# Kernel optimization log

Measured on AMD Instinct MI355X. Metric: run time of the kernel, lower is better.

## Reference

```python
import jax, jax.numpy as jnp
import numpy as np

B, LQ, C = 4, 4096, 384
NH, NL, NP = 6, 1, 4
HL, WL = 64, 64
LV = HL * WL
DH = C // NH
EPS = 1e-6


def layer_norm(x, g, b):
    mu = jnp.mean(x, axis=-1, keepdims=True)
    var = jnp.mean(jnp.square(x - mu), axis=-1, keepdims=True)
    return (x - mu) * jax.lax.rsqrt(var + EPS) * g + b


def ms_deform_attn_core(value, spatial_shapes, level_start_index, loc, attn_w):
    # value [B,LV,NH,DH]; loc [B,LQ,NH,NL,NP,2] in [0,1]; attn_w [B,LQ,NH,NL,NP]
    ss = np.asarray(spatial_shapes)
    lsi = np.asarray(level_start_index)
    Bv, _, nH, dh = value.shape
    Lq = loc.shape[1]
    nP = loc.shape[4]
    out = jnp.zeros((Bv, Lq, nH, dh), value.dtype)
    for l in range(loc.shape[3]):
        Hl, Wl = int(ss[l, 0]), int(ss[l, 1])
        st = int(lsi[l])
        vflat = value[:, st:st + Hl * Wl]  # [B, Hl*Wl, nH, dh]
        xy = loc[:, :, :, l]               # [B,LQ,nH,NP,2]
        # grid_sample(align_corners=False): pixel = loc * size - 0.5
        x = xy[..., 0] * Wl - 0.5
        y = xy[..., 1] * Hl - 0.5
        x0 = jnp.floor(x)
        y0 = jnp.floor(y)
        wx = x - x0
        wy = y - y0
        x0i = x0.astype(jnp.int32)
        y0i = y0.astype(jnp.int32)

        def gather(xi, yi):
            # zero padding outside the feature map (padding_mode='zeros')
            valid = (xi >= 0) & (xi < Wl) & (yi >= 0) & (yi < Hl)
            idx = jnp.clip(yi, 0, Hl - 1) * Wl + jnp.clip(xi, 0, Wl - 1)  # [B,LQ,nH,NP]
            idx2 = idx.transpose(0, 1, 3, 2).reshape(Bv, Lq * nP, nH)
            g = jnp.take_along_axis(vflat, idx2[..., None], axis=1)       # [B,LQ*NP,nH,dh]
            g = g.reshape(Bv, Lq, nP, nH, dh).transpose(0, 1, 3, 2, 4)    # [B,LQ,nH,NP,dh]
            return g * valid[..., None].astype(value.dtype)

        samp = (gather(x0i, y0i) * ((1 - wx) * (1 - wy))[..., None]
                + gather(x0i + 1, y0i) * (wx * (1 - wy))[..., None]
                + gather(x0i, y0i + 1) * ((1 - wx) * wy)[..., None]
                + gather(x0i + 1, y0i + 1) * (wx * wy)[..., None])
        out = out + jnp.einsum('bqhpd,bqhp->bqhd', samp, attn_w[:, :, :, l])
    return out.reshape(Bv, Lq, nH * dh)


def setup_inputs() -> dict:
    key = jax.random.key(0)
    ks = jax.random.split(key, 12)
    s = 0.02
    return {
        'query': jax.random.normal(ks[0], (B, LQ, C), jnp.float32),
        'reference_points': jax.random.uniform(ks[1], (B, LQ, NL, 2), dtype=jnp.float32),
        'feat': jax.random.normal(ks[2], (B, LV, C), jnp.float32),
        'spatial_shapes': jnp.array([[HL, WL]], jnp.int32),
        'level_start_index': jnp.array([0], jnp.int32),
        'ln_q_g': jnp.ones((C,), jnp.float32), 'ln_q_b': jnp.zeros((C,), jnp.float32),
        'ln_f_g': jnp.ones((C,), jnp.float32), 'ln_f_b': jnp.zeros((C,), jnp.float32),
        'gamma': jax.random.normal(ks[3], (C,), jnp.float32) * 0.1,
        'Wv': jax.random.normal(ks[4], (C, C), jnp.float32) * s,
        'bv': jnp.zeros((C,), jnp.float32),
        'Wo': jax.random.normal(ks[5], (C, NH * NL * NP * 2), jnp.float32) * s,
        'bo': jax.random.normal(ks[6], (NH * NL * NP * 2,), jnp.float32) * 0.5,
        'Wa': jax.random.normal(ks[7], (C, NH * NL * NP), jnp.float32) * s,
        'ba': jnp.zeros((NH * NL * NP,), jnp.float32),
        'Wout': jax.random.normal(ks[8], (C, C), jnp.float32) * s,
        'bout': jnp.zeros((C,), jnp.float32),
    }


def reference(query, reference_points, feat, spatial_shapes, level_start_index,
              ln_q_g, ln_q_b, ln_f_g, ln_f_b, gamma,
              Wv, bv, Wo, bo, Wa, ba, Wout, bout):
    q = layer_norm(query, ln_q_g, ln_q_b)
    f = layer_norm(feat, ln_f_g, ln_f_b)
    value = (f @ Wv + bv).reshape(B, LV, NH, DH)
    offsets = (q @ Wo + bo).reshape(B, LQ, NH, NL, NP, 2)
    attn_w = jax.nn.softmax((q @ Wa + ba).reshape(B, LQ, NH, NL * NP), axis=-1)
    attn_w = attn_w.reshape(B, LQ, NH, NL, NP)
    # offset normalizer is (W, H) per level
    norm = jnp.stack([spatial_shapes[:, 1], spatial_shapes[:, 0]], -1).astype(jnp.float32)
    loc = reference_points[:, :, None, :, None, :] + offsets / norm[None, None, None, :, None, :]
    attn = ms_deform_attn_core(value, spatial_shapes, level_start_index, loc, attn_w)
    attn = attn @ Wout + bout
    return query + gamma * attn
```

## Files before the change

### kernel.cpp

```cpp
#include <hip/hip_runtime.h>
#include <math.h>

#define B_    4
#define LQ_   4096
#define C_    384
#define NH_   6
#define NP_   4
#define HL_   64
#define WL_   64
#define LV_   (HL_ * WL_)
#define ROWS_ (B_ * LQ_)
#define EPS_  1e-6f
#define NOFF_ 48
#define NLOG_ 24

typedef unsigned short u16;
typedef __bf16 bf16x8 __attribute__((ext_vector_type(8)));
typedef float  f32x4  __attribute__((ext_vector_type(4)));

__device__ __forceinline__ float bf2f(u16 v) {
    unsigned int u = ((unsigned int)v) << 16;
    return __uint_as_float(u);
}
__device__ __forceinline__ u16 f2bf(float f) {
    unsigned int u = __float_as_uint(f);
    u += 0x7fff + ((u >> 16) & 1);
    return (u16)(u >> 16);
}

__device__ __forceinline__ f32x4 mfma16(bf16x8 a, bf16x8 b, f32x4 c) {
    return __builtin_amdgcn_mfma_f32_16x16x32_bf16(a, b, c, 0, 0, 0);
}

__device__ __forceinline__ void gl_lds16(const u16* g, u16* l) {
    __builtin_amdgcn_global_load_lds(
        (const __attribute__((address_space(1))) unsigned int*)g,
        (__attribute__((address_space(3))) unsigned int*)l, 16, 0, 0);
}

__global__ __launch_bounds__(256) void prep_weights(
    const float* __restrict__ Wv, const float* __restrict__ Wout,
    const float* __restrict__ Wo, const float* __restrict__ Wa,
    const float* __restrict__ bo, const float* __restrict__ ba,
    u16* __restrict__ WvT, u16* __restrict__ WoutT, u16* __restrict__ WcT,
    float* __restrict__ bias_c)
{
    const int KN = 384 * 384;
    int idx = blockIdx.x * 256 + threadIdx.x;
    if (idx < KN) {
        int n = idx / 384, k = idx - n * 384;
        WvT[idx] = f2bf(Wv[k * 384 + n]);
    } else if (idx < 2 * KN) {
        int t = idx - KN;
        int n = t / 384, k = t - n * 384;
        WoutT[t] = f2bf(Wout[k * 384 + n]);
    } else if (idx < 2 * KN + 80 * 384) {
        int t = idx - 2 * KN;
        int n = t / 384, k = t - n * 384;
        float v = (n < 48) ? Wo[k * 48 + n] : (n < 72 ? Wa[k * 24 + (n - 48)] : 0.f);
        WcT[t] = f2bf(v);
    } else if (idx < 2 * KN + 80 * 384 + 80) {
        int n = idx - (2 * KN + 80 * 384);
        bias_c[n] = (n < 48) ? bo[n] : (n < 72 ? ba[n - 48] : 0.f);
    }
}

__global__ __launch_bounds__(256) void ln_kernel(
    const float* __restrict__ query, const float* __restrict__ feat,
    const float* __restrict__ qg, const float* __restrict__ qb,
    const float* __restrict__ fg, const float* __restrict__ fb,
    u16* __restrict__ qout, u16* __restrict__ fout)
{
    int wid  = threadIdx.x >> 6;
    int lane = threadIdx.x & 63;
    int row  = blockIdx.x * 4 + wid;
    const float *src, *g, *bsh;
    u16* dst;
    int r;
    if (row < ROWS_) { src = query; g = qg; bsh = qb; dst = qout; r = row; }
    else             { src = feat;  g = fg; bsh = fb; dst = fout; r = row - ROWS_; }

    const float* x = src + (size_t)r * C_;
    float v[6];
    float s = 0.f;
#pragma unroll
    for (int k = 0; k < 6; ++k) { v[k] = x[lane + 64 * k]; s += v[k]; }
#pragma unroll
    for (int off = 32; off; off >>= 1) s += __shfl_xor(s, off);
    float mu = s * (1.f / C_);

    float s2 = 0.f;
#pragma unroll
    for (int k = 0; k < 6; ++k) { float d = v[k] - mu; s2 += d * d; }
#pragma unroll
    for (int off = 32; off; off >>= 1) s2 += __shfl_xor(s2, off);
    float rs = rsqrtf(s2 * (1.f / C_) + EPS_);

    u16* y = dst + (size_t)r * C_;
#pragma unroll
    for (int k = 0; k < 6; ++k) {
        int c = lane + 64 * k;
        y[c] = f2bf((v[k] - mu) * rs * g[c] + bsh[c]);
    }
}

template<int MODE>
__global__ __launch_bounds__(256) void mfma_gemm(
    const u16* __restrict__ A, const u16* __restrict__ Bt,
    const float* __restrict__ bias, const float* __restrict__ resid,
    const float* __restrict__ gamma, void* __restrict__ Cout)
{
    const int K = 384, N = 384;
    __shared__ __align__(16) u16 As[128 * 32];
    __shared__ __align__(16) u16 Bs[128 * 32];

    int tid  = threadIdx.x;
    int lane = tid & 63, wid = tid >> 6;
    int m0 = blockIdx.y * 128, n0 = blockIdx.x * 128;
    int wm = (wid >> 1) * 64, wn = (wid & 1) * 64;
    int fr = lane & 15, quad = lane >> 4;

    int srow = tid >> 2;
    int scol = (tid & 3) * 8;
    const u16* agp0 = A  + (size_t)(m0 + srow) * K + scol;
    const u16* agp1 = A  + (size_t)(m0 + srow + 64) * K + scol;
    const u16* bgp0 = Bt + (size_t)(n0 + srow) * K + scol;
    const u16* bgp1 = Bt + (size_t)(n0 + srow + 64) * K + scol;
    u16* al0 = As + tid * 8;  u16* al1 = As + 2048 + tid * 8;
    u16* bl0 = Bs + tid * 8;  u16* bl1 = Bs + 2048 + tid * 8;

    f32x4 zero = {0.f, 0.f, 0.f, 0.f};
    f32x4 acc[4][4];
#pragma unroll
    for (int i = 0; i < 4; ++i)
#pragma unroll
        for (int j = 0; j < 4; ++j) acc[i][j] = zero;

    for (int k0 = 0; k0 < K; k0 += 32) {
        gl_lds16(agp0 + k0, al0);
        gl_lds16(agp1 + k0, al1);
        gl_lds16(bgp0 + k0, bl0);
        gl_lds16(bgp1 + k0, bl1);
        __syncthreads();
        bf16x8 af[4], bfr[4];
#pragma unroll
        for (int i = 0; i < 4; ++i)
            af[i] = *(bf16x8*)&As[(wm + i * 16 + fr) * 32 + quad * 8];
#pragma unroll
        for (int j = 0; j < 4; ++j)
            bfr[j] = *(bf16x8*)&Bs[(wn + j * 16 + fr) * 32 + quad * 8];
#pragma unroll
        for (int i = 0; i < 4; ++i)
#pragma unroll
            for (int j = 0; j < 4; ++j)
                acc[i][j] = mfma16(af[i], bfr[j], acc[i][j]);
        __syncthreads();
    }

#pragma unroll
    for (int i = 0; i < 4; ++i) {
        int row = m0 + wm + i * 16 + quad * 4;
#pragma unroll
        for (int j = 0; j < 4; ++j) {
            int col = n0 + wn + j * 16 + fr;
            float bcol = bias[col];
#pragma unroll
            for (int r = 0; r < 4; ++r) {
                float v = acc[i][j][r] + bcol;
                size_t o = (size_t)(row + r) * N + col;
                if (MODE == 0) ((u16*)Cout)[o] = f2bf(v);
                else ((float*)Cout)[o] = resid[o] + gamma[col] * v;
            }
        }
    }
}

__global__ __launch_bounds__(256) void mfma_small(
    const u16* __restrict__ A, const u16* __restrict__ Bt,
    const float* __restrict__ bias,
    float* __restrict__ offs, float* __restrict__ logits)
{
    const int K = 384;
    __shared__ __align__(16) u16 Bs[80 * 384];
    __shared__ __align__(16) u16 As[64 * 32];

    int tid  = threadIdx.x;
    int lane = tid & 63, wid = tid >> 6;
    int m0 = blockIdx.x * 64;
    int fr = lane & 15, quad = lane >> 4;

    for (int i = tid; i < 3840; i += 256)
        ((float4*)Bs)[i] = ((const float4*)Bt)[i];

    int srow = tid >> 2, scol = (tid & 3) * 8;
    const u16* agp = A + (size_t)(m0 + srow) * K + scol;
    u16* al = As + tid * 8;

    f32x4 zero = {0.f, 0.f, 0.f, 0.f};
    f32x4 acc[5];
#pragma unroll
    for (int j = 0; j < 5; ++j) acc[j] = zero;

    __syncthreads();

    for (int k0 = 0; k0 < K; k0 += 32) {
        gl_lds16(agp + k0, al);
        __syncthreads();
        bf16x8 af = *(bf16x8*)&As[(wid * 16 + fr) * 32 + quad * 8];
#pragma unroll
        for (int j = 0; j < 5; ++j) {
            bf16x8 bf = *(bf16x8*)&Bs[(j * 16 + fr) * 384 + k0 + quad * 8];
            acc[j] = mfma16(af, bf, acc[j]);
        }
        __syncthreads();
    }

    int row = m0 + wid * 16 + quad * 4;
#pragma unroll
    for (int j = 0; j < 5; ++j) {
        int col = j * 16 + fr;
        if (col < 72) {
            float bcol = bias[col];
#pragma unroll
            for (int r = 0; r < 4; ++r) {
                float v = acc[j][r] + bcol;
                if (col < 48) offs[(size_t)(row + r) * NOFF_ + col] = v;
                else          logits[(size_t)(row + r) * NLOG_ + (col - 48)] = v;
            }
        }
    }
}

__global__ __launch_bounds__(384) void sample_kernel(
    const u16*  __restrict__ value,
    const float* __restrict__ rp,
    const float* __restrict__ offs,
    const float* __restrict__ logits,
    u16* __restrict__ attn)
{
    __shared__ float w_s[NH_][NP_][4];
    __shared__ int   pos_s[NH_][NP_][4];

    int bq = blockIdx.x;
    int b  = bq / LQ_;
    int t  = threadIdx.x;

    if (t < NLOG_) {
        int h = t >> 2, p = t & 3;
        const float* lg = logits + (size_t)bq * NLOG_ + h * 4;
        float l0 = lg[0], l1 = lg[1], l2 = lg[2], l3 = lg[3];
        float mx = fmaxf(fmaxf(l0, l1), fmaxf(l2, l3));
        float e0 = expf(l0 - mx), e1 = expf(l1 - mx), e2 = expf(l2 - mx), e3 = expf(l3 - mx);
        float den = e0 + e1 + e2 + e3;
        float ep = (p == 0) ? e0 : (p == 1) ? e1 : (p == 2) ? e2 : e3;
        float aw = ep / den;

        float rx = rp[(size_t)bq * 2 + 0];
        float ry = rp[(size_t)bq * 2 + 1];
        float ox = offs[(size_t)bq * NOFF_ + t * 2 + 0];
        float oy = offs[(size_t)bq * NOFF_ + t * 2 + 1];
        float x = (rx + ox * (1.0f / WL_)) * (float)WL_ - 0.5f;
        float y = (ry + oy * (1.0f / HL_)) * (float)HL_ - 0.5f;
        float x0f = floorf(x), y0f = floorf(y);
        float wx = x - x0f, wy = y - y0f;
        int x0 = (int)x0f, y0 = (int)y0f;
#pragma unroll
        for (int c = 0; c < 4; ++c) {
            int xi = x0 + (c & 1);
            int yi = y0 + (c >> 1);
            bool valid = (xi >= 0) && (xi < WL_) && (yi >= 0) && (yi < HL_);
            int xc = xi < 0 ? 0 : (xi > WL_ - 1 ? WL_ - 1 : xi);
            int yc = yi < 0 ? 0 : (yi > HL_ - 1 ? HL_ - 1 : yi);
            float wc = ((c & 1) ? wx : 1.f - wx) * ((c >> 1) ? wy : 1.f - wy);
            pos_s[h][p][c] = yc * WL_ + xc;
            w_s[h][p][c]   = valid ? wc * aw : 0.f;
        }
    }
    __syncthreads();

    int h = t >> 6, d = t & 63;
    const u16* vb = value + ((size_t)b * LV_) * C_ + h * 64 + d;
    float acc = 0.f;
#pragma unroll
    for (int p = 0; p < NP_; ++p) {
#pragma unroll
        for (int c = 0; c < 4; ++c) {
            acc += w_s[h][p][c] * bf2f(vb[(size_t)pos_s[h][p][c] * C_]);
        }
    }
    attn[(size_t)bq * C_ + t] = f2bf(acc);
}

extern "C" void kernel_launch(void* const* d_in, const int* in_sizes, int n_in,
                              void* d_out, int out_size, void* d_ws, size_t ws_size,
                              hipStream_t stream)
{
    const float* query  = (const float*)d_in[0];
    const float* rp     = (const float*)d_in[1];
    const float* feat   = (const float*)d_in[2];
    const float* gamma  = (const float*)d_in[9];
    const float* Wv     = (const float*)d_in[10];
    const float* bv     = (const float*)d_in[11];
    const float* Wo     = (const float*)d_in[12];
    const float* bo     = (const float*)d_in[13];
    const float* Wa     = (const float*)d_in[14];
    const float* ba     = (const float*)d_in[15];
    const float* Wout   = (const float*)d_in[16];
    const float* bout   = (const float*)d_in[17];
    float* out = (float*)d_out;

    u16* wsu    = (u16*)d_ws;
    u16* qb     = wsu;
    u16* fb     = qb    + (size_t)ROWS_ * C_;
    u16* valb   = fb    + (size_t)ROWS_ * C_;
    u16* attnb  = valb  + (size_t)ROWS_ * C_;
    u16* WvT    = attnb + (size_t)ROWS_ * C_;
    u16* WoutT  = WvT   + 384 * 384;
    u16* WcT    = WoutT + 384 * 384;
    float* offs   = (float*)(WcT + 80 * 384);
    float* logits = offs + (size_t)ROWS_ * NOFF_;
    float* bias_c = logits + (size_t)ROWS_ * NLOG_;

    prep_weights<<<1273, 256, 0, stream>>>(Wv, Wout, Wo, Wa, bo, ba,
                                           WvT, WoutT, WcT, bias_c);

    ln_kernel<<<8192, 256, 0, stream>>>(query, feat,
        (const float*)d_in[5], (const float*)d_in[6],
        (const float*)d_in[7], (const float*)d_in[8], qb, fb);

    mfma_gemm<0><<<dim3(3, 128), 256, 0, stream>>>(fb, WvT, bv, nullptr, nullptr, valb);

    mfma_small<<<256, 256, 0, stream>>>(qb, WcT, bias_c, offs, logits);

    sample_kernel<<<ROWS_, 384, 0, stream>>>(valb, rp, offs, logits, attnb);

    mfma_gemm<1><<<dim3(3, 128), 256, 0, stream>>>(attnb, WoutT, bout, query, gamma, out);
}
```

Measured before the change: 202.7 us.

## Fuse deformable sampling with output projection GEMM in one kernel

Replaces the per-query sampling kernel and the separate output-projection GEMM with one kernel. Each block takes 32 queries, computes softmax and sampling metadata into shared memory, and gathers value rows with 8-wide bf16 vector loads. The sampled rows stay in LDS and are multiplied by WoutT with MFMA, and the residual epilogue is applied in place. This removes the attn round-trip through global memory and one launch, but WoutT is read straight from global memory by every block with no LDS staging, and the grid is only 512 blocks.

```diff
diff --git a/kernel.cpp b/kernel.cpp
--- a/kernel.cpp
+++ b/kernel.cpp
@@ -104,11 +104,9 @@
     }
 }
 
-template<int MODE>
-__global__ __launch_bounds__(256) void mfma_gemm(
+__global__ __launch_bounds__(256) void mfma_gemm_value(
     const u16* __restrict__ A, const u16* __restrict__ Bt,
-    const float* __restrict__ bias, const float* __restrict__ resid,
-    const float* __restrict__ gamma, void* __restrict__ Cout)
+    const float* __restrict__ bias, u16* __restrict__ Cout)
 {
     const int K = 384, N = 384;
     __shared__ __align__(16) u16 As[128 * 32];
@@ -167,9 +165,7 @@
 #pragma unroll
             for (int r = 0; r < 4; ++r) {
                 float v = acc[i][j][r] + bcol;
-                size_t o = (size_t)(row + r) * N + col;
-                if (MODE == 0) ((u16*)Cout)[o] = f2bf(v);
-                else ((float*)Cout)[o] = resid[o] + gamma[col] * v;
+                Cout[(size_t)(row + r) * N + col] = f2bf(v);
             }
         }
     }
@@ -231,64 +227,135 @@
     }
 }
 
-__global__ __launch_bounds__(384) void sample_kernel(
+#define QT_   32
+#define APAD_ 392
+
+__global__ __launch_bounds__(256) void fused_sample_out(
     const u16*  __restrict__ value,
     const float* __restrict__ rp,
     const float* __restrict__ offs,
     const float* __restrict__ logits,
-    u16* __restrict__ attn)
-{
-    __shared__ float w_s[NH_][NP_][4];
-    __shared__ int   pos_s[NH_][NP_][4];
-
-    int bq = blockIdx.x;
-    int b  = bq / LQ_;
+    const u16*  __restrict__ WoutT,
+    const float* __restrict__ bout,
+    const float* __restrict__ gamma,
+    const float* __restrict__ query,
+    float* __restrict__ out)
+{
+    __shared__ float meta[QT_ * NH_ * NP_ * 4];
+    __shared__ __align__(16) u16 attn_s[QT_ * APAD_];
+
     int t  = threadIdx.x;
-
-    if (t < NLOG_) {
-        int h = t >> 2, p = t & 3;
-        const float* lg = logits + (size_t)bq * NLOG_ + h * 4;
+    int m0 = blockIdx.x * QT_;
+    int b  = m0 / LQ_;
+
+#pragma unroll
+    for (int j = 0; j < 3; ++j) {
+        int u = t + 256 * j;
+        int q = u / (NH_ * NP_);
+        int rem = u - q * (NH_ * NP_);
+        int h = rem >> 2, p = rem & 3;
+        int r = m0 + q;
+
+        const float* lg = logits + (size_t)r * NLOG_ + h * 4;
         float l0 = lg[0], l1 = lg[1], l2 = lg[2], l3 = lg[3];
         float mx = fmaxf(fmaxf(l0, l1), fmaxf(l2, l3));
-        float e0 = expf(l0 - mx), e1 = expf(l1 - mx), e2 = expf(l2 - mx), e3 = expf(l3 - mx);
+        float e0 = expf(l0 - mx), e1 = expf(l1 - mx);
+        float e2 = expf(l2 - mx), e3 = expf(l3 - mx);
         float den = e0 + e1 + e2 + e3;
         float ep = (p == 0) ? e0 : (p == 1) ? e1 : (p == 2) ? e2 : e3;
         float aw = ep / den;
 
-        float rx = rp[(size_t)bq * 2 + 0];
-        float ry = rp[(size_t)bq * 2 + 1];
-        float ox = offs[(size_t)bq * NOFF_ + t * 2 + 0];
-        float oy = offs[(size_t)bq * NOFF_ + t * 2 + 1];
-        float x = (rx + ox * (1.0f / WL_)) * (float)WL_ - 0.5f;
-        float y = (ry + oy * (1.0f / HL_)) * (float)HL_ - 0.5f;
+        float rx = rp[(size_t)r * 2 + 0];
+        float ry = rp[(size_t)r * 2 + 1];
+        float ox = offs[(size_t)r * NOFF_ + (h * 4 + p) * 2 + 0];
+        float oy = offs[(size_t)r * NOFF_ + (h * 4 + p) * 2 + 1];
+        float x = rx * (float)WL_ + ox - 0.5f;
+        float y = ry * (float)HL_ + oy - 0.5f;
         float x0f = floorf(x), y0f = floorf(y);
-        float wx = x - x0f, wy = y - y0f;
         int x0 = (int)x0f, y0 = (int)y0f;
-#pragma unroll
-        for (int c = 0; c < 4; ++c) {
-            int xi = x0 + (c & 1);
-            int yi = y0 + (c >> 1);
-            bool valid = (xi >= 0) && (xi < WL_) && (yi >= 0) && (yi < HL_);
-            int xc = xi < 0 ? 0 : (xi > WL_ - 1 ? WL_ - 1 : xi);
-            int yc = yi < 0 ? 0 : (yi > HL_ - 1 ? HL_ - 1 : yi);
-            float wc = ((c & 1) ? wx : 1.f - wx) * ((c >> 1) ? wy : 1.f - wy);
-            pos_s[h][p][c] = yc * WL_ + xc;
-            w_s[h][p][c]   = valid ? wc * aw : 0.f;
-        }
+
+        int midx = u * 4;
+        meta[midx + 0] = x - x0f;
+        meta[midx + 1] = y - y0f;
+        meta[midx + 2] = aw;
+        meta[midx + 3] = __int_as_float((y0 << 16) | (x0 & 0xffff));
     }
     __syncthreads();
 
-    int h = t >> 6, d = t & 63;
-    const u16* vb = value + ((size_t)b * LV_) * C_ + h * 64 + d;
-    float acc = 0.f;
-#pragma unroll
-    for (int p = 0; p < NP_; ++p) {
-#pragma unroll
-        for (int c = 0; c < 4; ++c) {
-            acc += w_s[h][p][c] * bf2f(vb[(size_t)pos_s[h][p][c] * C_]);
-        }
-    }
-    attn[(size_t)bq * C_ + t] = f2bf(acc);
+#pragma unroll
+    for (int j = 0; j < 6; ++j) {
+        int v = t + 256 * j;
+        int q = v / 48, dc = v - q * 48;
+        int h = dc >> 3;
+        int col0 = dc << 3;
+        const u16* vbase = value + (size_t)b * LV_ * C_ + col0;
+
+        float acc[8] = {0.f, 0.f, 0.f, 0.f, 0.f, 0.f, 0.f, 0.f};
+#pragma unroll
+        for (int p = 0; p < NP_; ++p) {
+            int midx = ((q * NH_ + h) * NP_ + p) * 4;
+            float wx = meta[midx + 0];
+            float wy = meta[midx + 1];
+            float aw = meta[midx + 2];
+            int packed = __float_as_int(meta[midx + 3]);
+            int x0 = (packed << 16) >> 16;
+            int y0 = packed >> 16;
+#pragma unroll
+            for (int c = 0; c < 4; ++c) {
+                int xi = x0 + (c & 1);
+                int yi = y0 + (c >> 1);
+                bool valid = (xi >= 0) && (xi < WL_) && (yi >= 0) && (yi < HL_);
+                int xc = xi < 0 ? 0 : (xi > WL_ - 1 ? WL_ - 1 : xi);
+                int yc = yi < 0 ? 0 : (yi > HL_ - 1 ? HL_ - 1 : yi);
+                float w = ((c & 1) ? wx : 1.f - wx) * ((c >> 1) ? wy : 1.f - wy) * aw;
+                w = valid ? w : 0.f;
+                bf16x8 vv = *(const bf16x8*)(vbase + (size_t)(yc * WL_ + xc) * C_);
+#pragma unroll
+                for (int e = 0; e < 8; ++e) acc[e] += w * (float)vv[e];
+            }
+        }
+        u16* dst = attn_s + q * APAD_ + col0;
+#pragma unroll
+        for (int e = 0; e < 8; ++e) dst[e] = f2bf(acc[e]);
+    }
+    __syncthreads();
+
+    int lane = t & 63, wid = t >> 6;
+    int fr = lane & 15, quad = lane >> 4;
+    int wn0 = wid * 96;
+
+    f32x4 zero = {0.f, 0.f, 0.f, 0.f};
+    f32x4 acc[2][6];
+#pragma unroll
+    for (int i = 0; i < 2; ++i)
+#pragma unroll
+        for (int j = 0; j < 6; ++j) acc[i][j] = zero;
+
+    for (int k0 = 0; k0 < 384; k0 += 32) {
+        bf16x8 a0 = *(bf16x8*)&attn_s[(fr)      * APAD_ + k0 + quad * 8];
+        bf16x8 a1 = *(bf16x8*)&attn_s[(16 + fr) * APAD_ + k0 + quad * 8];
+#pragma unroll
+        for (int nt = 0; nt < 6; ++nt) {
+            bf16x8 bb = *(const bf16x8*)(WoutT + (size_t)(wn0 + nt * 16 + fr) * 384 + k0 + quad * 8);
+            acc[0][nt] = mfma16(a0, bb, acc[0][nt]);
+            acc[1][nt] = mfma16(a1, bb, acc[1][nt]);
+        }
+    }
+
+#pragma unroll
+    for (int nt = 0; nt < 6; ++nt) {
+        int col = wn0 + nt * 16 + fr;
+        float g = gamma[col], bc = bout[col];
+#pragma unroll
+        for (int mt = 0; mt < 2; ++mt) {
+            int r0 = m0 + mt * 16 + quad * 4;
+#pragma unroll
+            for (int rr = 0; rr < 4; ++rr) {
+                size_t o = (size_t)(r0 + rr) * C_ + col;
+                out[o] = query[o] + g * (acc[mt][nt][rr] + bc);
+            }
+        }
+    }
 }
 
 extern "C" void kernel_launch(void* const* d_in, const int* in_sizes, int n_in,
@@ -313,8 +380,7 @@
     u16* qb     = wsu;
     u16* fb     = qb    + (size_t)ROWS_ * C_;
     u16* valb   = fb    + (size_t)ROWS_ * C_;
-    u16* attnb  = valb  + (size_t)ROWS_ * C_;
-    u16* WvT    = attnb + (size_t)ROWS_ * C_;
+    u16* WvT    = valb  + (size_t)ROWS_ * C_;
     u16* WoutT  = WvT   + 384 * 384;
     u16* WcT    = WoutT + 384 * 384;
     float* offs   = (float*)(WcT + 80 * 384);
@@ -328,11 +394,10 @@
         (const float*)d_in[5], (const float*)d_in[6],
         (const float*)d_in[7], (const float*)d_in[8], qb, fb);
 
-    mfma_gemm<0><<<dim3(3, 128), 256, 0, stream>>>(fb, WvT, bv, nullptr, nullptr, valb);
+    mfma_gemm_value<<<dim3(3, 128), 256, 0, stream>>>(fb, WvT, bv, valb);
 
     mfma_small<<<256, 256, 0, stream>>>(qb, WcT, bias_c, offs, logits);
 
-    sample_kernel<<<ROWS_, 384, 0, stream>>>(valb, rp, offs, logits, attnb);
-
-    mfma_gemm<1><<<dim3(3, 128), 256, 0, stream>>>(attnb, WoutT, bout, query, gamma, out);
-}
+    fused_sample_out<<<ROWS_ / QT_, 256, 0, stream>>>(
+        valb, rp, offs, logits, WoutT, bout, gamma, query, out);
+}
```

After: 190.6 us. 1.06x faster.
